# Optimization experiments

Hardware: AMD Instinct MI355X
Metric: run time of the kernel (lower is better)

The kernel has to match this reference:

```python
import jax, jax.numpy as jnp
import numpy as np

LEAKY_SLOPE = 0.01  # torch nn.LeakyReLU / F.leaky_relu default


def gcn_diffusion(adj, order, feat):
    # A_gcn = adj + I; sym-normalized diffusion D^-1/2 A D^-1/2 applied repeatedly
    B, N, _ = adj.shape
    A = adj + jnp.eye(N, dtype=adj.dtype)
    dinv_sqrt = jnp.sum(A, axis=2) ** -0.5  # [B, N]
    outs = []
    h = feat
    for _ in range(order):
        h = jnp.matmul(A, dinv_sqrt[..., None] * h) * dinv_sqrt[..., None]
        outs.append(h)
    return outs


def scattering_s4(adj, feat):
    # lazy random walk P = 1/2 (I + A D^-1); wavelets Psi_j = P^{2^{j-1}} - P^{2^j}
    dinv = 1.0 / jnp.sum(adj, axis=2)  # [B, N]
    p = feat
    us = []
    for _ in range(8):  # powers P^1 .. P^8
        p = 0.5 * p + 0.5 * jnp.matmul(adj, dinv[..., None] * p)
        us.append(p)
    h1 = feat - us[0]      # I - P
    h2 = us[0] - us[1]     # P - P^2
    h3 = us[1] - us[3]     # P^2 - P^4
    h4 = us[3] - us[7]     # P^4 - P^8
    return h1, h2, h3, h4


def sctconv(X, adj, W1, b1, W2, b2, a, moment):
    leaky = lambda x: jax.nn.leaky_relu(x, LEAKY_SLOPE)
    h = X  # [B, N, F]
    hA, hA2, hA3 = gcn_diffusion(adj, 3, X)
    hA, hA2, hA3 = leaky(hA), leaky(hA2), leaky(hA3)
    s1, s2, s3, s4 = scattering_s4(adj, X)
    mom = jnp.asarray(moment, dtype=X.dtype)
    s1 = jnp.abs(s1) ** mom
    s2 = jnp.abs(s2) ** mom
    s3 = jnp.abs(s3) ** mom
    s4 = jnp.abs(s4) ** mom
    # NOTE: original concatenates only (hA, hA2, s1..s4) -> 6 branches; hA3 is unused.
    h_all = jnp.stack([hA, hA2, s1, s2, s3, s4], axis=1)  # [B, 6, N, F]
    h_b = jnp.broadcast_to(h[:, None], h_all.shape)        # [B, 6, N, F]
    a_input = jnp.concatenate([h_b, h_all], axis=3)        # [B, 6, N, 2F]
    e = jnp.einsum('bknc,c->bkn', jax.nn.relu(a_input), a[:, 0])  # [B, 6, N]
    attention = jax.nn.softmax(e, axis=1)[..., None]       # [B, 6, N, 1]
    h_prime = jnp.mean(attention * h_all, axis=1)          # [B, N, F]
    out = leaky(h_prime @ W1.T + b1)
    out = leaky(out @ W2.T + b2)
    return out


def setup_inputs() -> dict:
    key = jax.random.key(0)
    kx, ka, k1, k2, k3, k4, k5 = jax.random.split(key, 7)
    B, N, F = 8, 4096, 64
    X = jax.random.normal(kx, (B, N, F), dtype=jnp.float32)
    adj = jax.random.uniform(ka, (B, N, N), dtype=jnp.float32)
    s = 1.0 / np.sqrt(F)
    W1 = jax.random.uniform(k1, (F, F), minval=-s, maxval=s, dtype=jnp.float32)
    b1 = jax.random.uniform(k2, (F,), minval=-s, maxval=s, dtype=jnp.float32)
    W2 = jax.random.uniform(k3, (F, F), minval=-s, maxval=s, dtype=jnp.float32)
    b2 = jax.random.uniform(k4, (F,), minval=-s, maxval=s, dtype=jnp.float32)
    a = jax.random.normal(k5, (2 * F, 1), dtype=jnp.float32) * 0.1
    return {"X": X, "adj": adj, "W1": W1, "b1": b1, "W2": W2, "b2": b2, "a": a, "moment": 1}


def reference(X, adj, W1, b1, W2, b2, a, moment):
    return sctconv(X, adj, W1, b1, W2, b2, a, moment)
```

## Files before the change

### kernel.cpp

```cpp
#include <hip/hip_runtime.h>
#include <hip/hip_bf16.h>
#include <cstdio>
#include <cstdint>

#define BB 8
#define NN 4096
#define FF 64

typedef __attribute__((ext_vector_type(8))) short bf16x8;
typedef __attribute__((ext_vector_type(4))) float f32x4;

__device__ __forceinline__ unsigned short f2bf(float f){
  unsigned int u = __float_as_uint(f);
  u += 0x7FFFu + ((u >> 16) & 1u);
  return (unsigned short)(u >> 16);
}

__device__ __forceinline__ float leaky01(float x){ return x > 0.f ? x : 0.01f * x; }

__global__ __launch_bounds__(256) void k_convert(const float* __restrict__ adj,
    unsigned short* __restrict__ At, float* __restrict__ dinv, float* __restrict__ dsq)
{
  const int bid = blockIdx.x;
  const int b = bid & 7, mt = bid >> 3, m0 = mt * 32;
  const int tid = threadIdx.x;
  const int r = tid >> 3, g = tid & 7;
  const float* src = adj + ((size_t)b * NN + m0 + r) * NN + ((g ^ (r & 7)) << 3);
  unsigned short* dst = At + (size_t)bid * 64 * 2048 + (tid << 3);
  float s = 0.f;
  for (int t = 0; t < 64; ++t){
    const float* p = src + t * 64;
    float4 a = *(const float4*)p;
    float4 c = *(const float4*)(p + 4);
    s += ((a.x + a.y) + (a.z + a.w)) + ((c.x + c.y) + (c.z + c.w));
    bf16x8 v;
    v[0] = (short)f2bf(a.x); v[1] = (short)f2bf(a.y); v[2] = (short)f2bf(a.z); v[3] = (short)f2bf(a.w);
    v[4] = (short)f2bf(c.x); v[5] = (short)f2bf(c.y); v[6] = (short)f2bf(c.z); v[7] = (short)f2bf(c.w);
    *(bf16x8*)(dst + (size_t)t * 2048) = v;
  }
  s += __shfl_xor(s, 1); s += __shfl_xor(s, 2); s += __shfl_xor(s, 4);
  if (g == 0){
    dinv[(size_t)b * NN + m0 + r] = 1.0f / s;
    dsq [(size_t)b * NN + m0 + r] = 1.0f / sqrtf(s + 1.0f);
  }
}

__global__ __launch_bounds__(256) void k_prep(const float* __restrict__ X,
    const float* __restrict__ dinv, const float* __restrict__ dsq,
    unsigned short* __restrict__ vt)
{
  const int b = blockIdx.y, n0 = blockIdx.x * 64, tid = threadIdx.x;
  __shared__ unsigned short tg[64][65], ts[64][65];
  #pragma unroll
  for (int i = 0; i < 4; ++i){
    int idx = i * 256 + tid, n = idx >> 4, c4 = (idx & 15) * 4;
    size_t rb = (size_t)b * NN + n0 + n;
    float4 x = *(const float4*)(X + rb * 64 + c4);
    float di = dinv[b * NN + n0 + n], dv = dsq[b * NN + n0 + n];
    tg[c4 + 0][n] = f2bf(dv * x.x); tg[c4 + 1][n] = f2bf(dv * x.y);
    tg[c4 + 2][n] = f2bf(dv * x.z); tg[c4 + 3][n] = f2bf(dv * x.w);
    ts[c4 + 0][n] = f2bf(di * x.x); ts[c4 + 1][n] = f2bf(di * x.y);
    ts[c4 + 2][n] = f2bf(di * x.z); ts[c4 + 3][n] = f2bf(di * x.w);
  }
  __syncthreads();
  #pragma unroll
  for (int i = 0; i < 4; ++i){
    int idx = i * 256 + tid, c = idx >> 4, n4 = (idx & 15) * 4;
    *(ushort4*)(vt + ((size_t)b * 128 + c) * NN + n0 + n4) =
        make_ushort4(tg[c][n4], tg[c][n4 + 1], tg[c][n4 + 2], tg[c][n4 + 3]);
    *(ushort4*)(vt + ((size_t)b * 128 + 64 + c) * NN + n0 + n4) =
        make_ushort4(ts[c][n4], ts[c][n4 + 1], ts[c][n4 + 2], ts[c][n4 + 3]);
  }
}

template<int NC>
__global__ __launch_bounds__(256, 4) void k_gemm_fused(
    const unsigned short* __restrict__ At,
    const unsigned short* __restrict__ vtR, int c0,
    const float* __restrict__ sprev, float* __restrict__ P, float* __restrict__ snap,
    const float* __restrict__ dinv, int writeVtS,
    const float* __restrict__ gprev, float* __restrict__ gout,
    const float* __restrict__ dsq, int writeVtG,
    unsigned short* __restrict__ vtW)
{
  constexpr int NF = NC / 64;
  constexpr int BI = NC / 32;
  __shared__ __align__(16) unsigned short As[2][32 * 64];
  __shared__ __align__(16) unsigned short Bs[2][NC * 64];
  const int bid = blockIdx.x;
  const int b = bid & 7, mt = bid >> 3, m0 = mt * 32;
  const int tid = threadIdx.x;
  const int w = tid >> 6, l = tid & 63;
  const unsigned short* Atile = At + (size_t)bid * 64 * 2048;
  const unsigned short* Bg = vtR + ((size_t)b * 128 + c0) * NN;

  auto stage = [&](int buf, int t){
    {
      const unsigned short* gp = Atile + (size_t)t * 2048 + (tid << 3);
      __builtin_amdgcn_global_load_lds((const __attribute__((address_space(1))) void*)gp,
          (__attribute__((address_space(3))) void*)(&As[buf][tid << 3]), 16, 0, 0);
    }
    #pragma unroll
    for (int i = 0; i < BI; ++i){
      int idx = i * 256 + tid, c = idx >> 3, g = idx & 7;
      const unsigned short* gp = Bg + (size_t)c * NN + t * 64 + ((g ^ (c & 7)) << 3);
      __builtin_amdgcn_global_load_lds((const __attribute__((address_space(1))) void*)gp,
          (__attribute__((address_space(3))) void*)(&Bs[buf][idx << 3]), 16, 0, 0);
    }
  };

  f32x4 acc[2][NF];
  #pragma unroll
  for (int mi = 0; mi < 2; ++mi)
    #pragma unroll
    for (int ni = 0; ni < NF; ++ni)
      #pragma unroll
      for (int j = 0; j < 4; ++j) acc[mi][ni][j] = 0.f;

  stage(0, 0);
  const int r0 = l & 15, hq = l >> 4, sw = r0 & 7;
  constexpr int NT = NN / 64;
  for (int t = 0; t < NT; ++t){
    const int cur = t & 1;
    if (t + 1 < NT){
      stage(cur ^ 1, t + 1);
      if constexpr (NC == 128) asm volatile("s_waitcnt vmcnt(5)" ::: "memory");
      else                     asm volatile("s_waitcnt vmcnt(3)" ::: "memory");
    } else {
      asm volatile("s_waitcnt vmcnt(0)" ::: "memory");
    }
    __builtin_amdgcn_s_barrier();
    asm volatile("" ::: "memory");
    #pragma unroll
    for (int kk = 0; kk < 2; ++kk){
      const int g8 = ((kk * 4 + hq) ^ sw) << 3;
      bf16x8 af[2], bfr[NF];
      #pragma unroll
      for (int mi = 0; mi < 2; ++mi)
        af[mi] = *(const bf16x8*)&As[cur][(mi * 16 + r0) * 64 + g8];
      #pragma unroll
      for (int ni = 0; ni < NF; ++ni)
        bfr[ni] = *(const bf16x8*)&Bs[cur][(w * 16 * NF + ni * 16 + r0) * 64 + g8];
      #pragma unroll
      for (int mi = 0; mi < 2; ++mi)
        #pragma unroll
        for (int ni = 0; ni < NF; ++ni)
          acc[mi][ni] = __builtin_amdgcn_mfma_f32_16x16x32_bf16(af[mi], bfr[ni], acc[mi][ni], 0, 0, 0);
    }
    asm volatile("" ::: "memory");
    __builtin_amdgcn_s_barrier();
    asm volatile("" ::: "memory");
  }

  const bool isScat = (NC == 64) || (w >= 2);
  if (isScat){
    const int wS = (NC == 64) ? w : (w - 2);
    #pragma unroll
    for (int mi = 0; mi < 2; ++mi){
      const int rb = m0 + mi * 16 + hq * 4;
      const size_t rowb = (size_t)b * NN + rb;
      float4 dv4 = *(const float4*)(dinv + (size_t)b * NN + rb);
      #pragma unroll
      for (int ni = 0; ni < NF; ++ni){
        const int cs = wS * 16 * NF + ni * 16 + r0;
        float pn[4];
        #pragma unroll
        for (int j = 0; j < 4; ++j){
          float pv = sprev[(rowb + j) * 64 + cs];
          pn[j] = 0.5f * (pv + acc[mi][ni][j]);
          P[(rowb + j) * 64 + cs] = pn[j];
        }
        if (snap){
          #pragma unroll
          for (int j = 0; j < 4; ++j) snap[(rowb + j) * 64 + cs] = pn[j];
        }
        if (writeVtS){
          ushort4 vv = make_ushort4(f2bf(dv4.x * pn[0]), f2bf(dv4.y * pn[1]),
                                    f2bf(dv4.z * pn[2]), f2bf(dv4.w * pn[3]));
          *(ushort4*)(vtW + ((size_t)b * 128 + 64 + cs) * NN + rb) = vv;
        }
      }
    }
  }
  if constexpr (NC == 128){
    if (!isScat){
      #pragma unroll
      for (int mi = 0; mi < 2; ++mi){
        const int rb = m0 + mi * 16 + hq * 4;
        const size_t rowb = (size_t)b * NN + rb;
        float4 dq4 = *(const float4*)(dsq + (size_t)b * NN + rb);
        #pragma unroll
        for (int ni = 0; ni < NF; ++ni){
          const int cg = w * 16 * NF + ni * 16 + r0;
          float hn[4];
          const float dq[4] = {dq4.x, dq4.y, dq4.z, dq4.w};
          #pragma unroll
          for (int j = 0; j < 4; ++j){
            float hv = gprev[(rowb + j) * 64 + cg];
            hn[j] = (acc[mi][ni][j] + dq[j] * hv) * dq[j];
            gout[(rowb + j) * 64 + cg] = hn[j];
          }
          if (writeVtG){
            ushort4 vv = make_ushort4(f2bf(dq[0] * hn[0]), f2bf(dq[1] * hn[1]),
                                      f2bf(dq[2] * hn[2]), f2bf(dq[3] * hn[3]));
            *(ushort4*)(vtW + ((size_t)b * 128 + cg) * NN + rb) = vv;
          }
        }
      }
    }
  }
}

__global__ __launch_bounds__(256) void k_attn(
    const float* __restrict__ X,  const float* __restrict__ hA, const float* __restrict__ hA2,
    const float* __restrict__ U1, const float* __restrict__ U2, const float* __restrict__ U4,
    const float* __restrict__ U8, const float* __restrict__ W1, const float* __restrict__ b1,
    const float* __restrict__ W2, const float* __restrict__ b2, const float* __restrict__ av,
    const int* __restrict__ momp, float* __restrict__ out)
{
  __shared__ float W1s[64][65], W2s[64][65];
  __shared__ float a1s[64], a2s[64], b1s[64], b2s[64];
  __shared__ float hp[4][64], o1[4][64];
  const int tid = threadIdx.x;
  for (int e = tid; e < 4096; e += 256){
    W1s[e >> 6][e & 63] = W1[e];
    W2s[e >> 6][e & 63] = W2[e];
  }
  if (tid < 64){ a1s[tid] = av[tid]; a2s[tid] = av[64 + tid]; b1s[tid] = b1[tid]; b2s[tid] = b2[tid]; }
  __syncthreads();
  const int w = tid >> 6, l = tid & 63;
  size_t row = (size_t)blockIdx.x * 4 + w;
  size_t off = row * 64 + l;
  float x  = X[off];
  float u1 = U1[off], u2 = U2[off], u4 = U4[off], u8 = U8[off];
  float br[6];
  br[0] = leaky01(hA[off]);
  br[1] = leaky01(hA2[off]);
  float d1 = fabsf(x - u1), d2 = fabsf(u1 - u2), d3 = fabsf(u2 - u4), d4 = fabsf(u4 - u8);
  int mom = *momp;
  if (mom == 1){ br[2] = d1; br[3] = d2; br[4] = d3; br[5] = d4; }
  else {
    float m = (float)mom;
    br[2] = powf(d1, m); br[3] = powf(d2, m); br[4] = powf(d3, m); br[5] = powf(d4, m);
  }
  float v = fmaxf(x, 0.f) * a1s[l];
  for (int o = 32; o; o >>= 1) v += __shfl_xor(v, o);
  float base = v;
  float e[6];
  #pragma unroll
  for (int k = 0; k < 6; ++k){
    float t = fmaxf(br[k], 0.f) * a2s[l];
    for (int o = 32; o; o >>= 1) t += __shfl_xor(t, o);
    e[k] = base + t;
  }
  float mx = e[0];
  #pragma unroll
  for (int k = 1; k < 6; ++k) mx = fmaxf(mx, e[k]);
  float s = 0.f, att[6];
  #pragma unroll
  for (int k = 0; k < 6; ++k){ att[k] = expf(e[k] - mx); s += att[k]; }
  float inv = 1.0f / (6.0f * s);
  float hpv = 0.f;
  #pragma unroll
  for (int k = 0; k < 6; ++k) hpv += att[k] * br[k];
  hpv *= inv;
  hp[w][l] = hpv;
  __syncthreads();
  float acc = b1s[l];
  #pragma unroll 8
  for (int c = 0; c < 64; ++c) acc += hp[w][c] * W1s[l][c];
  o1[w][l] = leaky01(acc);
  __syncthreads();
  float acc2 = b2s[l];
  #pragma unroll 8
  for (int c = 0; c < 64; ++c) acc2 += o1[w][c] * W2s[l][c];
  out[off] = leaky01(acc2);
}

static constexpr size_t OFF_ADJB = 0;
static constexpr size_t OFF_VTA  = OFF_ADJB + (size_t)BB * NN * NN * 2;
static constexpr size_t OFF_VTB  = OFF_VTA  + (size_t)BB * 128 * NN * 2;
static constexpr size_t OFF_HA   = OFF_VTB  + (size_t)BB * 128 * NN * 2;
static constexpr size_t OFF_HA2  = OFF_HA   + (size_t)BB * NN * 64 * 4;
static constexpr size_t OFF_P    = OFF_HA2  + (size_t)BB * NN * 64 * 4;
static constexpr size_t OFF_U1   = OFF_P    + (size_t)BB * NN * 64 * 4;
static constexpr size_t OFF_U2   = OFF_U1   + (size_t)BB * NN * 64 * 4;
static constexpr size_t OFF_U4   = OFF_U2   + (size_t)BB * NN * 64 * 4;
static constexpr size_t OFF_U8   = OFF_U4   + (size_t)BB * NN * 64 * 4;
static constexpr size_t OFF_DINV = OFF_U8   + (size_t)BB * NN * 64 * 4;
static constexpr size_t OFF_DS   = OFF_DINV + (size_t)BB * NN * 4;
static constexpr size_t WS_NEED  = OFF_DS   + (size_t)BB * NN * 4;

extern "C" void kernel_launch(void* const* d_in, const int* in_sizes, int n_in,
                              void* d_out, int out_size, void* d_ws, size_t ws_size,
                              hipStream_t stream)
{
  const float* X   = (const float*)d_in[0];
  const float* adj = (const float*)d_in[1];
  const float* W1  = (const float*)d_in[2];
  const float* b1  = (const float*)d_in[3];
  const float* W2  = (const float*)d_in[4];
  const float* b2  = (const float*)d_in[5];
  const float* av  = (const float*)d_in[6];
  const int*  momp = (const int*)d_in[7];
  float* out = (float*)d_out;

  if (ws_size < WS_NEED){
    fprintf(stderr, "kernel_launch: workspace too small: %zu < %zu\n", ws_size, WS_NEED);
    return;
  }
  char* w = (char*)d_ws;
  unsigned short* At  = (unsigned short*)(w + OFF_ADJB);
  unsigned short* vtA = (unsigned short*)(w + OFF_VTA);
  unsigned short* vtB = (unsigned short*)(w + OFF_VTB);
  float* hA   = (float*)(w + OFF_HA);
  float* hA2  = (float*)(w + OFF_HA2);
  float* P    = (float*)(w + OFF_P);
  float* U1   = (float*)(w + OFF_U1);
  float* U2   = (float*)(w + OFF_U2);
  float* U4   = (float*)(w + OFF_U4);
  float* U8   = (float*)(w + OFF_U8);
  float* dinv = (float*)(w + OFF_DINV);
  float* dsq  = (float*)(w + OFF_DS);

  k_convert<<<1024, 256, 0, stream>>>(adj, At, dinv, dsq);
  dim3 tg64(NN / 64, BB);
  k_prep<<<tg64, 256, 0, stream>>>(X, dinv, dsq, vtA);

  k_gemm_fused<128><<<1024, 256, 0, stream>>>(At, vtA, 0,
      X, P, U1, dinv, 1, X, hA, dsq, 1, vtB);
  k_gemm_fused<128><<<1024, 256, 0, stream>>>(At, vtB, 0,
      P, P, U2, dinv, 1, hA, hA2, dsq, 0, vtA);
  unsigned short* vr = vtA;
  unsigned short* vw = vtB;
  for (int k = 3; k <= 8; ++k){
    float* snap = (k == 4) ? U4 : nullptr;
    float* pdst = (k == 8) ? U8 : P;
    k_gemm_fused<64><<<1024, 256, 0, stream>>>(At, vr, 64,
        P, pdst, snap, dinv, (k < 8) ? 1 : 0, nullptr, nullptr, nullptr, 0, vw);
    unsigned short* t = vr; vr = vw; vw = t;
  }

  k_attn<<<BB * NN / 4, 256, 0, stream>>>(X, hA, hA2, U1, U2, U4, U8,
                                          W1, b1, W2, b2, av, momp, out);
}
```

Measured before the change: 772.9 us.

## Triple-buffer GEMM staging and coalesce adjacency conversion through LDS

```diff
diff --git a/kernel.cpp b/kernel.cpp
--- a/kernel.cpp
+++ b/kernel.cpp
@@ -21,22 +21,32 @@
 __global__ __launch_bounds__(256) void k_convert(const float* __restrict__ adj,
     unsigned short* __restrict__ At, float* __restrict__ dinv, float* __restrict__ dsq)
 {
+  __shared__ unsigned short lt[32][264];
   const int bid = blockIdx.x;
   const int b = bid & 7, mt = bid >> 3, m0 = mt * 32;
   const int tid = threadIdx.x;
   const int r = tid >> 3, g = tid & 7;
-  const float* src = adj + ((size_t)b * NN + m0 + r) * NN + ((g ^ (r & 7)) << 3);
-  unsigned short* dst = At + (size_t)bid * 64 * 2048 + (tid << 3);
+  const int gs = (g ^ (r & 7)) << 3;
+  unsigned short* dst = At + (size_t)bid * (64 * 2048);
   float s = 0.f;
-  for (int t = 0; t < 64; ++t){
-    const float* p = src + t * 64;
-    float4 a = *(const float4*)p;
-    float4 c = *(const float4*)(p + 4);
-    s += ((a.x + a.y) + (a.z + a.w)) + ((c.x + c.y) + (c.z + c.w));
-    bf16x8 v;
-    v[0] = (short)f2bf(a.x); v[1] = (short)f2bf(a.y); v[2] = (short)f2bf(a.z); v[3] = (short)f2bf(a.w);
-    v[4] = (short)f2bf(c.x); v[5] = (short)f2bf(c.y); v[6] = (short)f2bf(c.z); v[7] = (short)f2bf(c.w);
-    *(bf16x8*)(dst + (size_t)t * 2048) = v;
+  for (int cc = 0; cc < 16; ++cc){
+    #pragma unroll
+    for (int rep = 0; rep < 8; ++rep){
+      int idx = rep * 256 + tid;
+      int rr = idx >> 6, c4 = (idx & 63) << 2;
+      float4 v = *(const float4*)(adj + ((size_t)b * NN + m0 + rr) * NN + cc * 256 + c4);
+      *(ushort4*)&lt[rr][c4] = make_ushort4(f2bf(v.x), f2bf(v.y), f2bf(v.z), f2bf(v.w));
+    }
+    __syncthreads();
+    #pragma unroll
+    for (int t = 0; t < 4; ++t){
+      bf16x8 v = *(const bf16x8*)&lt[r][t * 64 + gs];
+      #pragma unroll
+      for (int j = 0; j < 8; ++j)
+        s += __uint_as_float(((unsigned)(unsigned short)v[j]) << 16);
+      *(bf16x8*)(dst + (size_t)(cc * 4 + t) * 2048 + tid * 8) = v;
+    }
+    __syncthreads();
   }
   s += __shfl_xor(s, 1); s += __shfl_xor(s, 2); s += __shfl_xor(s, 4);
   if (g == 0){
@@ -74,7 +84,7 @@
 }
 
 template<int NC>
-__global__ __launch_bounds__(256, 4) void k_gemm_fused(
+__global__ __launch_bounds__(256, NC == 128 ? 2 : 4) void k_gemm_fused(
     const unsigned short* __restrict__ At,
     const unsigned short* __restrict__ vtR, int c0,
     const float* __restrict__ sprev, float* __restrict__ P, float* __restrict__ snap,
@@ -85,8 +95,8 @@
 {
   constexpr int NF = NC / 64;
   constexpr int BI = NC / 32;
-  __shared__ __align__(16) unsigned short As[2][32 * 64];
-  __shared__ __align__(16) unsigned short Bs[2][NC * 64];
+  __shared__ __align__(16) unsigned short As[3][32 * 64];
+  __shared__ __align__(16) unsigned short Bs[3][NC * 64];
   const int bid = blockIdx.x;
   const int b = bid & 7, mt = bid >> 3, m0 = mt * 32;
   const int tid = threadIdx.x;
@@ -118,12 +128,16 @@
       for (int j = 0; j < 4; ++j) acc[mi][ni][j] = 0.f;
 
   stage(0, 0);
+  stage(1, 1);
   const int r0 = l & 15, hq = l >> 4, sw = r0 & 7;
   constexpr int NT = NN / 64;
+  int cur = 0, nxt2 = 2;
   for (int t = 0; t < NT; ++t){
-    const int cur = t & 1;
-    if (t + 1 < NT){
-      stage(cur ^ 1, t + 1);
+    if (t + 2 < NT){
+      stage(nxt2, t + 2);
+      if constexpr (NC == 128) asm volatile("s_waitcnt vmcnt(10)" ::: "memory");
+      else                     asm volatile("s_waitcnt vmcnt(6)" ::: "memory");
+    } else if (t + 1 < NT){
       if constexpr (NC == 128) asm volatile("s_waitcnt vmcnt(5)" ::: "memory");
       else                     asm volatile("s_waitcnt vmcnt(3)" ::: "memory");
     } else {
@@ -150,6 +164,8 @@
     asm volatile("" ::: "memory");
     __builtin_amdgcn_s_barrier();
     asm volatile("" ::: "memory");
+    cur = (cur == 2) ? 0 : cur + 1;
+    nxt2 = (nxt2 == 2) ? 0 : nxt2 + 1;
   }
 
   const bool isScat = (NC == 64) || (w >= 2);
```

Result: slower. 816.2 us (+5.6%).

## Fuse six scattering diffusion steps into one cooperative persistent kernel

Applied to the files above, without the earlier changes.

```diff
diff --git a/kernel.cpp b/kernel.cpp
--- a/kernel.cpp
+++ b/kernel.cpp
@@ -1,7 +1,10 @@
 #include <hip/hip_runtime.h>
 #include <hip/hip_bf16.h>
+#include <hip/hip_cooperative_groups.h>
 #include <cstdio>
 #include <cstdint>
+
+namespace cg = cooperative_groups;
 
 #define BB 8
 #define NN 4096
@@ -211,6 +214,106 @@
   }
 }
 
+__global__ __launch_bounds__(256, 4) void k_scat6(
+    const unsigned short* __restrict__ At,
+    unsigned short* __restrict__ vtA, unsigned short* __restrict__ vtB,
+    float* __restrict__ Pb, float* __restrict__ U4b, float* __restrict__ U8b,
+    const float* __restrict__ dinv)
+{
+  cg::grid_group grid = cg::this_grid();
+  __shared__ __align__(16) unsigned short As[2][32 * 64];
+  __shared__ __align__(16) unsigned short Bs[2][64 * 64];
+  const int bid = blockIdx.x;
+  const int b = bid & 7, mt = bid >> 3, m0 = mt * 32;
+  const int tid = threadIdx.x;
+  const int w = tid >> 6, l = tid & 63;
+  const unsigned short* Atile = At + (size_t)bid * 64 * 2048;
+  const int r0 = l & 15, hq = l >> 4, sw = r0 & 7;
+
+  auto stageA = [&](int buf, int t){
+    const unsigned short* gp = Atile + (size_t)t * 2048 + (tid << 3);
+    __builtin_amdgcn_global_load_lds((const __attribute__((address_space(1))) void*)gp,
+        (__attribute__((address_space(3))) void*)(&As[buf][tid << 3]), 16, 0, 0);
+  };
+  auto stageB = [&](const unsigned short* Bg, int buf, int t){
+    #pragma unroll
+    for (int i = 0; i < 2; ++i){
+      int idx = i * 256 + tid, c = idx >> 3, g = idx & 7;
+      const unsigned short* gp = Bg + (size_t)c * NN + t * 64 + ((g ^ (c & 7)) << 3);
+      __builtin_amdgcn_global_load_lds((const __attribute__((address_space(1))) void*)gp,
+          (__attribute__((address_space(3))) void*)(&Bs[buf][idx << 3]), 16, 0, 0);
+    }
+  };
+
+  stageA(0, 0); stageA(1, 1);
+  for (int pp = 0; pp < 6; ++pp){
+    const unsigned short* vr = (pp & 1) ? vtB : vtA;
+    unsigned short* vw = (pp & 1) ? vtA : vtB;
+    const unsigned short* Bg = vr + ((size_t)b * 128 + 64) * NN;
+    stageB(Bg, 0, 0); stageB(Bg, 1, 1);
+
+    f32x4 acc[2];
+    #pragma unroll
+    for (int mi = 0; mi < 2; ++mi)
+      #pragma unroll
+      for (int j = 0; j < 4; ++j) acc[mi][j] = 0.f;
+
+    for (int t = 0; t < 64; ++t){
+      const int cur = t & 1;
+      if (t == 0)       asm volatile("s_waitcnt vmcnt(2)" ::: "memory");
+      else if (t < 63)  asm volatile("s_waitcnt vmcnt(3)" ::: "memory");
+      else              asm volatile("s_waitcnt vmcnt(0)" ::: "memory");
+      __builtin_amdgcn_s_barrier();
+      asm volatile("" ::: "memory");
+      #pragma unroll
+      for (int kk = 0; kk < 2; ++kk){
+        const int g8 = ((kk * 4 + hq) ^ sw) << 3;
+        bf16x8 af[2];
+        #pragma unroll
+        for (int mi = 0; mi < 2; ++mi)
+          af[mi] = *(const bf16x8*)&As[cur][(mi * 16 + r0) * 64 + g8];
+        bf16x8 bfr = *(const bf16x8*)&Bs[cur][(w * 16 + r0) * 64 + g8];
+        #pragma unroll
+        for (int mi = 0; mi < 2; ++mi)
+          acc[mi] = __builtin_amdgcn_mfma_f32_16x16x32_bf16(af[mi], bfr, acc[mi], 0, 0, 0);
+      }
+      asm volatile("" ::: "memory");
+      __builtin_amdgcn_s_barrier();
+      asm volatile("" ::: "memory");
+      if (t + 2 < 64){ stageA(cur, t + 2); stageB(Bg, cur, t + 2); }
+      else if (t == 63 && pp < 5){ stageA(0, 0); stageA(1, 1); }
+    }
+
+    float* pdst = (pp == 5) ? U8b : Pb;
+    float* snap = (pp == 1) ? U4b : nullptr;
+    const int wvt = (pp < 5);
+    #pragma unroll
+    for (int mi = 0; mi < 2; ++mi){
+      const int rb = m0 + mi * 16 + hq * 4;
+      const size_t rowb = (size_t)b * NN + rb;
+      float4 dv4 = *(const float4*)(dinv + (size_t)b * NN + rb);
+      const int cs = w * 16 + r0;
+      float pn[4];
+      #pragma unroll
+      for (int j = 0; j < 4; ++j){
+        float pv = Pb[(rowb + j) * 64 + cs];
+        pn[j] = 0.5f * (pv + acc[mi][j]);
+        pdst[(rowb + j) * 64 + cs] = pn[j];
+      }
+      if (snap){
+        #pragma unroll
+        for (int j = 0; j < 4; ++j) snap[(rowb + j) * 64 + cs] = pn[j];
+      }
+      if (wvt){
+        ushort4 vv = make_ushort4(f2bf(dv4.x * pn[0]), f2bf(dv4.y * pn[1]),
+                                  f2bf(dv4.z * pn[2]), f2bf(dv4.w * pn[3]));
+        *(ushort4*)(vw + ((size_t)b * 128 + 64 + cs) * NN + rb) = vv;
+      }
+    }
+    grid.sync();
+  }
+}
+
 __global__ __launch_bounds__(256) void k_attn(
     const float* __restrict__ X,  const float* __restrict__ hA, const float* __restrict__ hA2,
     const float* __restrict__ U1, const float* __restrict__ U2, const float* __restrict__ U4,
@@ -331,14 +434,21 @@
       X, P, U1, dinv, 1, X, hA, dsq, 1, vtB);
   k_gemm_fused<128><<<1024, 256, 0, stream>>>(At, vtB, 0,
       P, P, U2, dinv, 1, hA, hA2, dsq, 0, vtA);
-  unsigned short* vr = vtA;
-  unsigned short* vw = vtB;
-  for (int k = 3; k <= 8; ++k){
-    float* snap = (k == 4) ? U4 : nullptr;
-    float* pdst = (k == 8) ? U8 : P;
-    k_gemm_fused<64><<<1024, 256, 0, stream>>>(At, vr, 64,
-        P, pdst, snap, dinv, (k < 8) ? 1 : 0, nullptr, nullptr, nullptr, 0, vw);
-    unsigned short* t = vr; vr = vw; vw = t;
+
+  void* args[] = { (void*)&At, (void*)&vtA, (void*)&vtB,
+                   (void*)&P, (void*)&U4, (void*)&U8, (void*)&dinv };
+  hipError_t cerr = hipLaunchCooperativeKernel((const void*)k_scat6,
+      dim3(1024), dim3(256), args, 0, stream);
+  if (cerr != hipSuccess){
+    unsigned short* vr = vtA;
+    unsigned short* vw = vtB;
+    for (int k = 3; k <= 8; ++k){
+      float* snap = (k == 4) ? U4 : nullptr;
+      float* pdst = (k == 8) ? U8 : P;
+      k_gemm_fused<64><<<1024, 256, 0, stream>>>(At, vr, 64,
+          P, pdst, snap, dinv, (k < 8) ? 1 : 0, nullptr, nullptr, nullptr, 0, vw);
+      unsigned short* t = vr; vr = vw; vw = t;
+    }
   }
 
   k_attn<<<BB * NN / 4, 256, 0, stream>>>(X, hA, hA2, U1, U2, U4, U8,
```

After: 1.535 ms. 98.5% more time.

## Load GEMM operands directly into registers with multi-stage prefetch, dropping LDS staging

Applied to the files above, without the earlier changes.

```diff
diff --git a/kernel.cpp b/kernel.cpp
--- a/kernel.cpp
+++ b/kernel.cpp
@@ -25,7 +25,7 @@
   const int b = bid & 7, mt = bid >> 3, m0 = mt * 32;
   const int tid = threadIdx.x;
   const int r = tid >> 3, g = tid & 7;
-  const float* src = adj + ((size_t)b * NN + m0 + r) * NN + ((g ^ (r & 7)) << 3);
+  const float* src = adj + ((size_t)b * NN + m0 + r) * NN + (g << 3);
   unsigned short* dst = At + (size_t)bid * 64 * 2048 + (tid << 3);
   float s = 0.f;
   for (int t = 0; t < 64; ++t){
@@ -73,8 +73,18 @@
   }
 }
 
-template<int NC>
-__global__ __launch_bounds__(256, 4) void k_gemm_fused(
+#define LOADTILE(T, S) do {                                                     \
+    const int _t = (T);                                                         \
+    _Pragma("unroll") for (int _mi = 0; _mi < 2; ++_mi)                         \
+    _Pragma("unroll") for (int _kk = 0; _kk < 2; ++_kk)                         \
+      pa[S][_mi][_kk] = *(const bf16x8*)(Ab + (size_t)_t * 2048 + _mi * 1024 + _kk * 32); \
+    _Pragma("unroll") for (int _ni = 0; _ni < NF; ++_ni)                        \
+    _Pragma("unroll") for (int _kk = 0; _kk < 2; ++_kk)                         \
+      pb[S][_ni][_kk] = *(const bf16x8*)(Bb + (size_t)_ni * 65536 + _t * 64 + _kk * 32); \
+  } while (0)
+
+template<int NC, int DEPTH>
+__global__ __launch_bounds__(256, NC == 128 ? 4 : 3) void k_gemm_fused(
     const unsigned short* __restrict__ At,
     const unsigned short* __restrict__ vtR, int c0,
     const float* __restrict__ sprev, float* __restrict__ P, float* __restrict__ snap,
@@ -84,31 +94,16 @@
     unsigned short* __restrict__ vtW)
 {
   constexpr int NF = NC / 64;
-  constexpr int BI = NC / 32;
-  __shared__ __align__(16) unsigned short As[2][32 * 64];
-  __shared__ __align__(16) unsigned short Bs[2][NC * 64];
   const int bid = blockIdx.x;
   const int b = bid & 7, mt = bid >> 3, m0 = mt * 32;
   const int tid = threadIdx.x;
   const int w = tid >> 6, l = tid & 63;
-  const unsigned short* Atile = At + (size_t)bid * 64 * 2048;
-  const unsigned short* Bg = vtR + ((size_t)b * 128 + c0) * NN;
-
-  auto stage = [&](int buf, int t){
-    {
-      const unsigned short* gp = Atile + (size_t)t * 2048 + (tid << 3);
-      __builtin_amdgcn_global_load_lds((const __attribute__((address_space(1))) void*)gp,
-          (__attribute__((address_space(3))) void*)(&As[buf][tid << 3]), 16, 0, 0);
-    }
-    #pragma unroll
-    for (int i = 0; i < BI; ++i){
-      int idx = i * 256 + tid, c = idx >> 3, g = idx & 7;
-      const unsigned short* gp = Bg + (size_t)c * NN + t * 64 + ((g ^ (c & 7)) << 3);
-      __builtin_amdgcn_global_load_lds((const __attribute__((address_space(1))) void*)gp,
-          (__attribute__((address_space(3))) void*)(&Bs[buf][idx << 3]), 16, 0, 0);
-    }
-  };
-
+  const int r0 = l & 15, hq = l >> 4;
+  const unsigned short* Ab = At + (size_t)bid * (64 * 2048) + r0 * 64 + hq * 8;
+  const unsigned short* Bb = vtR + ((size_t)b * 128 + c0 + w * 16 * NF + r0) * NN + hq * 8;
+
+  bf16x8 pa[DEPTH][2][2];
+  bf16x8 pb[DEPTH][NF][2];
   f32x4 acc[2][NF];
   #pragma unroll
   for (int mi = 0; mi < 2; ++mi)
@@ -117,39 +112,24 @@
       #pragma unroll
       for (int j = 0; j < 4; ++j) acc[mi][ni][j] = 0.f;
 
-  stage(0, 0);
-  const int r0 = l & 15, hq = l >> 4, sw = r0 & 7;
-  constexpr int NT = NN / 64;
-  for (int t = 0; t < NT; ++t){
-    const int cur = t & 1;
-    if (t + 1 < NT){
-      stage(cur ^ 1, t + 1);
-      if constexpr (NC == 128) asm volatile("s_waitcnt vmcnt(5)" ::: "memory");
-      else                     asm volatile("s_waitcnt vmcnt(3)" ::: "memory");
-    } else {
-      asm volatile("s_waitcnt vmcnt(0)" ::: "memory");
+  #pragma unroll
+  for (int i = 0; i < DEPTH - 1; ++i) LOADTILE(i, i);
+
+  #pragma unroll 1
+  for (int tb = 0; tb < 64; tb += DEPTH){
+    #pragma unroll
+    for (int s = 0; s < DEPTH; ++s){
+      const int t = tb + s;
+      if (t + DEPTH - 1 < 64) LOADTILE(t + DEPTH - 1, (s + DEPTH - 1) % DEPTH);
+      #pragma unroll
+      for (int kk = 0; kk < 2; ++kk)
+        #pragma unroll
+        for (int mi = 0; mi < 2; ++mi)
+          #pragma unroll
+          for (int ni = 0; ni < NF; ++ni)
+            acc[mi][ni] = __builtin_amdgcn_mfma_f32_16x16x32_bf16(
+                pa[s][mi][kk], pb[s][ni][kk], acc[mi][ni], 0, 0, 0);
     }
-    __builtin_amdgcn_s_barrier();
-    asm volatile("" ::: "memory");
-    #pragma unroll
-    for (int kk = 0; kk < 2; ++kk){
-      const int g8 = ((kk * 4 + hq) ^ sw) << 3;
-      bf16x8 af[2], bfr[NF];
-      #pragma unroll
-      for (int mi = 0; mi < 2; ++mi)
-        af[mi] = *(const bf16x8*)&As[cur][(mi * 16 + r0) * 64 + g8];
-      #pragma unroll
-      for (int ni = 0; ni < NF; ++ni)
-        bfr[ni] = *(const bf16x8*)&Bs[cur][(w * 16 * NF + ni * 16 + r0) * 64 + g8];
-      #pragma unroll
-      for (int mi = 0; mi < 2; ++mi)
-        #pragma unroll
-        for (int ni = 0; ni < NF; ++ni)
-          acc[mi][ni] = __builtin_amdgcn_mfma_f32_16x16x32_bf16(af[mi], bfr[ni], acc[mi][ni], 0, 0, 0);
-    }
-    asm volatile("" ::: "memory");
-    __builtin_amdgcn_s_barrier();
-    asm volatile("" ::: "memory");
   }
 
   const bool isScat = (NC == 64) || (w >= 2);
@@ -327,16 +307,16 @@
   dim3 tg64(NN / 64, BB);
   k_prep<<<tg64, 256, 0, stream>>>(X, dinv, dsq, vtA);
 
-  k_gemm_fused<128><<<1024, 256, 0, stream>>>(At, vtA, 0,
+  k_gemm_fused<128, 2><<<1024, 256, 0, stream>>>(At, vtA, 0,
       X, P, U1, dinv, 1, X, hA, dsq, 1, vtB);
-  k_gemm_fused<128><<<1024, 256, 0, stream>>>(At, vtB, 0,
+  k_gemm_fused<128, 2><<<1024, 256, 0, stream>>>(At, vtB, 0,
       P, P, U2, dinv, 1, hA, hA2, dsq, 0, vtA);
   unsigned short* vr = vtA;
   unsigned short* vw = vtB;
   for (int k = 3; k <= 8; ++k){
     float* snap = (k == 4) ? U4 : nullptr;
     float* pdst = (k == 8) ? U8 : P;
-    k_gemm_fused<64><<<1024, 256, 0, stream>>>(At, vr, 64,
+    k_gemm_fused<64, 4><<<1024, 256, 0, stream>>>(At, vr, 64,
         P, pdst, snap, dinv, (k < 8) ? 1 : 0, nullptr, nullptr, nullptr, 0, vw);
     unsigned short* t = vr; vr = vw; vw = t;
   }
```

Measured after the change: 1.720 ms. 2.22x slower.
